# Performance work log

Hardware: AMD Instinct MI355X
Metric: run time of the kernel (lower is better)

The kernel has to match this reference:

```python
import jax, jax.numpy as jnp
import numpy as np

B, N, C, H = 4, 2048, 256, 16
D = C // H  # head dim = 16


def setup_inputs() -> dict:
    key = jax.random.key(0)
    k1, k2, k3 = jax.random.split(key, 3)
    x = jax.random.normal(k1, (B, N, C), dtype=jnp.float32)
    w_qkv = jax.random.normal(k2, (C, 3 * C), dtype=jnp.float32) * (C ** -0.5)
    b_qkv = jnp.zeros((3 * C,), dtype=jnp.float32)
    w_proj = jax.random.normal(k3, (C, C), dtype=jnp.float32) * (C ** -0.5)
    b_proj = jnp.zeros((C,), dtype=jnp.float32)
    return {"x": x, "w_qkv": w_qkv, "b_qkv": b_qkv, "w_proj": w_proj, "b_proj": b_proj}


def reference(x, w_qkv, b_qkv, w_proj, b_proj):
    b, n, c = x.shape
    qkv = x @ w_qkv + b_qkv                       # (B, N, 3C)
    qkv = qkv.reshape(b, n, 3, H, D)
    q = jnp.transpose(qkv[:, :, 0], (0, 2, 1, 3))  # (B, H, N, D)
    k = jnp.transpose(qkv[:, :, 1], (0, 2, 1, 3))
    v = jnp.transpose(qkv[:, :, 2], (0, 2, 1, 3))
    # NOTE: the original module applies NO 1/sqrt(d) scaling.
    attn = jnp.einsum('bhqd,bhkd->bhqk', q, k)     # (B, H, N, N)
    attn = jax.nn.softmax(attn, axis=-1)
    out = jnp.einsum('bhqk,bhkd->bhqd', attn, v)   # (B, H, N, D)
    out = jnp.transpose(out, (0, 2, 1, 3)).reshape(b, n, c)
    return out @ w_proj + b_proj
```

## Files before the change

kernel.cpp:

```cpp
#include <hip/hip_runtime.h>
#include <stdint.h>

typedef __attribute__((ext_vector_type(8))) short short8;
typedef __attribute__((ext_vector_type(4))) short short4v;
typedef __attribute__((ext_vector_type(4))) float float4v;
typedef __attribute__((ext_vector_type(16))) float float16v;
typedef __attribute__((ext_vector_type(4))) uint32_t uint4v;

__device__ __forceinline__ short f2bf(float f) {
    union { float f; uint32_t u; } v; v.f = f;
    uint32_t u = v.u;
    uint32_t r = (u + 0x7fffu + ((u >> 16) & 1u)) >> 16;
    return (short)r;
}

#if __has_builtin(__builtin_amdgcn_cvt_pk_bf16_f32)
typedef __bf16 bf16x2_t __attribute__((ext_vector_type(2)));
__device__ __forceinline__ uint32_t cvt_pk2(float a, float b) {
    union { bf16x2_t v; uint32_t u; } c;
    c.v = __builtin_amdgcn_cvt_pk_bf16_f32(a, b);
    return c.u;
}
#else
__device__ __forceinline__ uint32_t cvt_pk2(float a, float b) {
    union { float f; uint32_t u; } x, y; x.f = a; y.f = b;
    return ((x.u + 0x8000u) >> 16) | ((y.u + 0x8000u) & 0xFFFF0000u);
}
#endif


__global__ __launch_bounds__(256) void cvtW_kernel(const float* __restrict__ wqkv,
                                                   const float* __restrict__ wproj,
                                                   short* __restrict__ outq,
                                                   short* __restrict__ outp) {
    int idx = blockIdx.x * 256 + threadIdx.x;
    if (idx < 196608) {
        int n = idx >> 8, k = idx & 255;
        outq[idx] = f2bf(wqkv[k * 768 + n]);
    } else {
        int i = idx - 196608;
        int n = i >> 8, k = i & 255;
        outp[i] = f2bf(wproj[k * 256 + n]);
    }
}


template<int MODE>
__global__ __launch_bounds__(256) void gemm_kernel(
    const void* __restrict__ Ap, const short* __restrict__ Bt,
    const float* __restrict__ bias,
    short* __restrict__ outQ, short* __restrict__ outK, short* __restrict__ outV,
    float* __restrict__ outP)
{
    const int K = 256;
    int m0 = blockIdx.x * 64;
    int n0 = blockIdx.y * 64;
    int tid = threadIdx.x;
    int wave = tid >> 6, lane = tid & 63, quad = lane >> 4, lc = lane & 15;

    __shared__ __align__(16) short As[64 * 48];
    __shared__ __align__(16) short Bs[64 * 48];

    float4v acc[4];
    #pragma unroll
    for (int t = 0; t < 4; ++t) acc[t] = (float4v){0.f, 0.f, 0.f, 0.f};

    int srow = tid >> 2, sseg = tid & 3;

    for (int c = 0; c < K; c += 32) {
        __syncthreads();
        if (MODE == 0) {
            const float* src = (const float*)Ap + (size_t)(m0 + srow) * K + c + sseg * 8;
            float4 f0 = *(const float4*)src;
            float4 f1 = *(const float4*)(src + 4);
            uint4v u; u.x = cvt_pk2(f0.x, f0.y); u.y = cvt_pk2(f0.z, f0.w);
            u.z = cvt_pk2(f1.x, f1.y); u.w = cvt_pk2(f1.z, f1.w);
            *(uint4v*)(&As[srow * 48 + sseg * 8]) = u;
        } else {
            *(short8*)(&As[srow * 48 + sseg * 8]) =
                *(const short8*)((const short*)Ap + (size_t)(m0 + srow) * K + c + sseg * 8);
        }
        *(short8*)(&Bs[srow * 48 + sseg * 8]) =
            *(const short8*)(Bt + (size_t)(n0 + srow) * K + c + sseg * 8);
        __syncthreads();

        short8 af = *(short8*)(&As[(wave * 16 + lc) * 48 + quad * 8]);
        #pragma unroll
        for (int t = 0; t < 4; ++t) {
            short8 bf = *(short8*)(&Bs[(t * 16 + lc) * 48 + quad * 8]);
            acc[t] = __builtin_amdgcn_mfma_f32_16x16x32_bf16(af, bf, acc[t], 0, 0, 0);
        }
    }

    #pragma unroll
    for (int t = 0; t < 4; ++t) {
        int cg = n0 + t * 16 + lc;
        float bv = bias[cg];
        #pragma unroll
        for (int r = 0; r < 4; ++r) {
            int rg = m0 + wave * 16 + quad * 4 + r;
            float val = acc[t][r] + bv;
            if (MODE == 0) {
                int sq = cg >> 8, rem = cg & 255, h = rem >> 4, d = rem & 15;
                int b = rg >> 11, n = rg & 2047;
                if (sq == 0) val *= 1.4426950408889634f;
                short* dst = (sq == 0) ? outQ : ((sq == 1) ? outK : outV);
                dst[((((size_t)b * 16 + h) * 2048 + n) << 4) + d] = f2bf(val);
            } else {
                outP[(size_t)rg * 256 + cg] = val;
            }
        }
    }
}


__global__ __launch_bounds__(256) void attn_kernel(
    const short* __restrict__ Q, const short* __restrict__ Kp, const short* __restrict__ V,
    short* __restrict__ Out)
{
    const int N = 2048;
    int bh = blockIdx.y;
    int b = bh >> 4, h = bh & 15;
    int tid = threadIdx.x;
    int wave = tid >> 6, lane = tid & 63;
    int m = lane & 31, hi = lane >> 5;
    int qbase = blockIdx.x * 128 + wave * 32;

    const short* Qh = Q + (size_t)bh * N * 16;
    const short* Kh = Kp + (size_t)bh * N * 16;
    const short* Vh = V + (size_t)bh * N * 16;

    __shared__ __align__(16) short Vt[16][264];

    short8 qf = *(const short8*)(Qh + (size_t)(qbase + m) * 16 + hi * 8);

    short8 ones, zeros;
    #pragma unroll
    for (int j = 0; j < 8; ++j) { ones[j] = (short)0x3F80; zeros[j] = 0; }

    float16v Oacc, zf;
    #pragma unroll
    for (int j = 0; j < 16; ++j) { Oacc[j] = 0.f; zf[j] = 0.f; }

    int sd = tid & 15, sa = tid >> 4;
    int kb = ((sa & 1) << 3) | (((sa >> 1) & 1) << 2) | ((sa >> 2) << 4);

    short4v vpack[4];
    #pragma unroll
    for (int cc = 0; cc < 4; ++cc) {
        const short* vp = Vh + (size_t)(cc * 64 + kb) * 16 + sd;
        vpack[cc].x = vp[0]; vpack[cc].y = vp[16];
        vpack[cc].z = vp[32]; vpack[cc].w = vp[48];
    }

    short8 kf1 = *(const short8*)(Kh + (size_t)m * 16 + hi * 8);
    short8 kf2 = *(const short8*)(Kh + (size_t)(32 + m) * 16 + hi * 8);

    for (int sc = 0; sc < N; sc += 256) {
        __syncthreads();
        #pragma unroll
        for (int cc = 0; cc < 4; ++cc)
            *(short4v*)(&Vt[sd][cc * 64 + sa * 4]) = vpack[cc];
        if (sc + 256 < N) {
            #pragma unroll
            for (int cc = 0; cc < 4; ++cc) {
                const short* vp = Vh + (size_t)(sc + 256 + cc * 64 + kb) * 16 + sd;
                vpack[cc].x = vp[0]; vpack[cc].y = vp[16];
                vpack[cc].z = vp[32]; vpack[cc].w = vp[48];
            }
        }
        __syncthreads();

        #pragma unroll
        for (int it = 0; it < 4; ++it) {
            int c = sc + it * 64;
            int cn = (c + 64) & (N - 1);

            float16v S1 = __builtin_amdgcn_mfma_f32_32x32x16_bf16(kf1, qf, zf, 0, 0, 0);
            float16v S2 = __builtin_amdgcn_mfma_f32_32x32x16_bf16(kf2, qf, zf, 0, 0, 0);

            kf1 = *(const short8*)(Kh + (size_t)(cn + m) * 16 + hi * 8);
            kf2 = *(const short8*)(Kh + (size_t)(cn + 32 + m) * 16 + hi * 8);

            union { uint4v u; short8 s; } pA, pB, pC, pD;
            pA.u = (uint4v){
                cvt_pk2(__builtin_amdgcn_exp2f(S1[0]), __builtin_amdgcn_exp2f(S1[1])),
                cvt_pk2(__builtin_amdgcn_exp2f(S1[2]), __builtin_amdgcn_exp2f(S1[3])),
                cvt_pk2(__builtin_amdgcn_exp2f(S1[4]), __builtin_amdgcn_exp2f(S1[5])),
                cvt_pk2(__builtin_amdgcn_exp2f(S1[6]), __builtin_amdgcn_exp2f(S1[7]))};
            pB.u = (uint4v){
                cvt_pk2(__builtin_amdgcn_exp2f(S1[8]),  __builtin_amdgcn_exp2f(S1[9])),
                cvt_pk2(__builtin_amdgcn_exp2f(S1[10]), __builtin_amdgcn_exp2f(S1[11])),
                cvt_pk2(__builtin_amdgcn_exp2f(S1[12]), __builtin_amdgcn_exp2f(S1[13])),
                cvt_pk2(__builtin_amdgcn_exp2f(S1[14]), __builtin_amdgcn_exp2f(S1[15]))};
            pC.u = (uint4v){
                cvt_pk2(__builtin_amdgcn_exp2f(S2[0]), __builtin_amdgcn_exp2f(S2[1])),
                cvt_pk2(__builtin_amdgcn_exp2f(S2[2]), __builtin_amdgcn_exp2f(S2[3])),
                cvt_pk2(__builtin_amdgcn_exp2f(S2[4]), __builtin_amdgcn_exp2f(S2[5])),
                cvt_pk2(__builtin_amdgcn_exp2f(S2[6]), __builtin_amdgcn_exp2f(S2[7]))};
            pD.u = (uint4v){
                cvt_pk2(__builtin_amdgcn_exp2f(S2[8]),  __builtin_amdgcn_exp2f(S2[9])),
                cvt_pk2(__builtin_amdgcn_exp2f(S2[10]), __builtin_amdgcn_exp2f(S2[11])),
                cvt_pk2(__builtin_amdgcn_exp2f(S2[12]), __builtin_amdgcn_exp2f(S2[13])),
                cvt_pk2(__builtin_amdgcn_exp2f(S2[14]), __builtin_amdgcn_exp2f(S2[15]))};

            #pragma unroll
            for (int p = 0; p < 4; ++p) {
                short8 vf;
                if (m < 16)      vf = *(const short8*)(&Vt[m][it * 64 + p * 16 + hi * 8]);
                else if (m == 16) vf = ones;
                else              vf = zeros;
                short8 pf = (p == 0) ? pA.s : (p == 1) ? pB.s : (p == 2) ? pC.s : pD.s;
                Oacc = __builtin_amdgcn_mfma_f32_32x32x16_bf16(vf, pf, Oacc, 0, 0, 0);
            }
        }
    }

    float Lq = __shfl(Oacc[8], m, 64);
    float inv = 1.0f / Lq;
    uint32_t o0 = cvt_pk2(Oacc[0] * inv, Oacc[1] * inv);
    uint32_t o1 = cvt_pk2(Oacc[2] * inv, Oacc[3] * inv);
    uint32_t o2 = cvt_pk2(Oacc[4] * inv, Oacc[5] * inv);
    uint32_t o3 = cvt_pk2(Oacc[6] * inv, Oacc[7] * inv);
    short* row = Out + ((size_t)(b * 2048 + qbase + m)) * 256 + h * 16;
    uint2 w0; w0.x = o0; w0.y = o1;
    uint2 w1; w1.x = o2; w1.y = o3;
    *(uint2*)(row + hi * 4) = w0;
    *(uint2*)(row + 8 + hi * 4) = w1;
}


extern "C" void kernel_launch(void* const* d_in, const int* in_sizes, int n_in,
                              void* d_out, int out_size, void* d_ws, size_t ws_size,
                              hipStream_t stream) {
    const float* x      = (const float*)d_in[0];
    const float* w_qkv  = (const float*)d_in[1];
    const float* b_qkv  = (const float*)d_in[2];
    const float* w_proj = (const float*)d_in[3];
    const float* b_proj = (const float*)d_in[4];
    float* out = (float*)d_out;

    short* wqkvT  = (short*)d_ws;
    short* wprojT = wqkvT + 196608;
    short* Qb     = wprojT + 65536;
    short* Kb     = Qb + 2097152;
    short* Vb     = Kb + 2097152;
    short* Ab     = Vb + 2097152;

    cvtW_kernel<<<1024, 256, 0, stream>>>(w_qkv, w_proj, wqkvT, wprojT);

    gemm_kernel<0><<<dim3(128, 12), 256, 0, stream>>>(x, wqkvT, b_qkv, Qb, Kb, Vb, nullptr);

    attn_kernel<<<dim3(16, 64), 256, 0, stream>>>(Qb, Kb, Vb, Ab);

    gemm_kernel<1><<<dim3(128, 4), 256, 0, stream>>>(Ab, wprojT, b_proj,
                                                     nullptr, nullptr, nullptr, out);
}
```

Baseline: 132.9 us.

## Split attention key range across two wave groups and reduce partial outputs in LDS

The attention block grows to 512 threads, with two groups of four waves each processing half of the key sequence for the same 128 queries. The partial outputs and row sums are combined through shared memory before normalisation. The ones/zeros rows of the V tile are now stored in LDS instead of being chosen per lane, which removes branching in the inner loop. This doubles the waves per block to hide latency, at the cost of an extra reduction, more LDS, and two more barriers.

```diff
diff --git a/kernel.cpp b/kernel.cpp
--- a/kernel.cpp
+++ b/kernel.cpp
@@ -114,57 +114,64 @@
 }
 
 
-__global__ __launch_bounds__(256) void attn_kernel(
+__global__ __launch_bounds__(512, 8) void attn_kernel(
     const short* __restrict__ Q, const short* __restrict__ Kp, const short* __restrict__ V,
     short* __restrict__ Out)
 {
-    const int N = 2048;
+    const int NH = 1024;
     int bh = blockIdx.y;
     int b = bh >> 4, h = bh & 15;
     int tid = threadIdx.x;
     int wave = tid >> 6, lane = tid & 63;
     int m = lane & 31, hi = lane >> 5;
-    int qbase = blockIdx.x * 128 + wave * 32;
-
-    const short* Qh = Q + (size_t)bh * N * 16;
-    const short* Kh = Kp + (size_t)bh * N * 16;
-    const short* Vh = V + (size_t)bh * N * 16;
-
-    __shared__ __align__(16) short Vt[16][264];
+    int grp = wave >> 2;
+    int koff = grp << 10;
+    int qbase = blockIdx.x * 128 + (wave & 3) * 32;
+
+    const short* Qh = Q + (size_t)bh * 2048 * 16;
+    const short* Kh = Kp + (size_t)bh * 2048 * 16;
+    const short* Vh = V + (size_t)bh * 2048 * 16;
+
+    __shared__ __align__(16) short Vt[2][32][264];
+
+    for (int idx = tid; idx < 2 * 16 * 264; idx += 512) {
+        int buf = idx / (16 * 264);
+        int rem = idx - buf * (16 * 264);
+        int row = 16 + rem / 264;
+        int col = rem - (row - 16) * 264;
+        Vt[buf][row][col] = (row == 16) ? (short)0x3F80 : (short)0;
+    }
 
     short8 qf = *(const short8*)(Qh + (size_t)(qbase + m) * 16 + hi * 8);
 
-    short8 ones, zeros;
-    #pragma unroll
-    for (int j = 0; j < 8; ++j) { ones[j] = (short)0x3F80; zeros[j] = 0; }
-
     float16v Oacc, zf;
     #pragma unroll
     for (int j = 0; j < 16; ++j) { Oacc[j] = 0.f; zf[j] = 0.f; }
 
-    int sd = tid & 15, sa = tid >> 4;
+    int t8 = tid & 255;
+    int sd = t8 & 15, sa = t8 >> 4;
     int kb = ((sa & 1) << 3) | (((sa >> 1) & 1) << 2) | ((sa >> 2) << 4);
 
     short4v vpack[4];
     #pragma unroll
     for (int cc = 0; cc < 4; ++cc) {
-        const short* vp = Vh + (size_t)(cc * 64 + kb) * 16 + sd;
+        const short* vp = Vh + (size_t)(koff + cc * 64 + kb) * 16 + sd;
         vpack[cc].x = vp[0]; vpack[cc].y = vp[16];
         vpack[cc].z = vp[32]; vpack[cc].w = vp[48];
     }
 
-    short8 kf1 = *(const short8*)(Kh + (size_t)m * 16 + hi * 8);
-    short8 kf2 = *(const short8*)(Kh + (size_t)(32 + m) * 16 + hi * 8);
-
-    for (int sc = 0; sc < N; sc += 256) {
+    short8 kf1 = *(const short8*)(Kh + (size_t)(koff + m) * 16 + hi * 8);
+    short8 kf2 = *(const short8*)(Kh + (size_t)(koff + 32 + m) * 16 + hi * 8);
+
+    for (int sc = 0; sc < NH; sc += 256) {
         __syncthreads();
         #pragma unroll
         for (int cc = 0; cc < 4; ++cc)
-            *(short4v*)(&Vt[sd][cc * 64 + sa * 4]) = vpack[cc];
-        if (sc + 256 < N) {
+            *(short4v*)(&Vt[grp][sd][cc * 64 + sa * 4]) = vpack[cc];
+        if (sc + 256 < NH) {
             #pragma unroll
             for (int cc = 0; cc < 4; ++cc) {
-                const short* vp = Vh + (size_t)(sc + 256 + cc * 64 + kb) * 16 + sd;
+                const short* vp = Vh + (size_t)(koff + sc + 256 + cc * 64 + kb) * 16 + sd;
                 vpack[cc].x = vp[0]; vpack[cc].y = vp[16];
                 vpack[cc].z = vp[32]; vpack[cc].w = vp[48];
             }
@@ -174,13 +181,13 @@
         #pragma unroll
         for (int it = 0; it < 4; ++it) {
             int c = sc + it * 64;
-            int cn = (c + 64) & (N - 1);
+            int cn = (c + 64) & (NH - 1);
 
             float16v S1 = __builtin_amdgcn_mfma_f32_32x32x16_bf16(kf1, qf, zf, 0, 0, 0);
             float16v S2 = __builtin_amdgcn_mfma_f32_32x32x16_bf16(kf2, qf, zf, 0, 0, 0);
 
-            kf1 = *(const short8*)(Kh + (size_t)(cn + m) * 16 + hi * 8);
-            kf2 = *(const short8*)(Kh + (size_t)(cn + 32 + m) * 16 + hi * 8);
+            kf1 = *(const short8*)(Kh + (size_t)(koff + cn + m) * 16 + hi * 8);
+            kf2 = *(const short8*)(Kh + (size_t)(koff + cn + 32 + m) * 16 + hi * 8);
 
             union { uint4v u; short8 s; } pA, pB, pC, pD;
             pA.u = (uint4v){
@@ -206,27 +213,43 @@
 
             #pragma unroll
             for (int p = 0; p < 4; ++p) {
-                short8 vf;
-                if (m < 16)      vf = *(const short8*)(&Vt[m][it * 64 + p * 16 + hi * 8]);
-                else if (m == 16) vf = ones;
-                else              vf = zeros;
+                short8 vf = *(short8*)(&Vt[grp][m][it * 64 + p * 16 + hi * 8]);
                 short8 pf = (p == 0) ? pA.s : (p == 1) ? pB.s : (p == 2) ? pC.s : pD.s;
                 Oacc = __builtin_amdgcn_mfma_f32_32x32x16_bf16(vf, pf, Oacc, 0, 0, 0);
             }
         }
     }
 
-    float Lq = __shfl(Oacc[8], m, 64);
-    float inv = 1.0f / Lq;
-    uint32_t o0 = cvt_pk2(Oacc[0] * inv, Oacc[1] * inv);
-    uint32_t o1 = cvt_pk2(Oacc[2] * inv, Oacc[3] * inv);
-    uint32_t o2 = cvt_pk2(Oacc[4] * inv, Oacc[5] * inv);
-    uint32_t o3 = cvt_pk2(Oacc[6] * inv, Oacc[7] * inv);
-    short* row = Out + ((size_t)(b * 2048 + qbase + m)) * 256 + h * 16;
-    uint2 w0; w0.x = o0; w0.y = o1;
-    uint2 w1; w1.x = o2; w1.y = o3;
-    *(uint2*)(row + hi * 4) = w0;
-    *(uint2*)(row + 8 + hi * 4) = w1;
+    __syncthreads();
+    float* cb = (float*)&Vt[0][0][0];
+    if (wave >= 4) {
+        int base = ((wave - 4) * 64 + lane) * 12;
+        *(float4v*)(cb + base)     = (float4v){Oacc[0], Oacc[1], Oacc[2], Oacc[3]};
+        *(float4v*)(cb + base + 4) = (float4v){Oacc[4], Oacc[5], Oacc[6], Oacc[7]};
+        cb[base + 8] = Oacc[8];
+    }
+    __syncthreads();
+    if (wave < 4) {
+        int base = (wave * 64 + lane) * 12;
+        float4v p0 = *(float4v*)(cb + base);
+        float4v p1 = *(float4v*)(cb + base + 4);
+        float Lp = cb[base + 8];
+        Oacc[0] += p0[0]; Oacc[1] += p0[1]; Oacc[2] += p0[2]; Oacc[3] += p0[3];
+        Oacc[4] += p1[0]; Oacc[5] += p1[1]; Oacc[6] += p1[2]; Oacc[7] += p1[3];
+        Oacc[8] += Lp;
+
+        float Lq = __shfl(Oacc[8], m, 64);
+        float inv = 1.0f / Lq;
+        uint32_t o0 = cvt_pk2(Oacc[0] * inv, Oacc[1] * inv);
+        uint32_t o1 = cvt_pk2(Oacc[2] * inv, Oacc[3] * inv);
+        uint32_t o2 = cvt_pk2(Oacc[4] * inv, Oacc[5] * inv);
+        uint32_t o3 = cvt_pk2(Oacc[6] * inv, Oacc[7] * inv);
+        short* row = Out + ((size_t)(b * 2048 + qbase + m)) * 256 + h * 16;
+        uint2 w0; w0.x = o0; w0.y = o1;
+        uint2 w1; w1.x = o2; w1.y = o3;
+        *(uint2*)(row + hi * 4) = w0;
+        *(uint2*)(row + 8 + hi * 4) = w1;
+    }
 }
 
 
@@ -251,7 +274,7 @@
 
     gemm_kernel<0><<<dim3(128, 12), 256, 0, stream>>>(x, wqkvT, b_qkv, Qb, Kb, Vb, nullptr);
 
-    attn_kernel<<<dim3(16, 64), 256, 0, stream>>>(Qb, Kb, Vb, Ab);
+    attn_kernel<<<dim3(16, 64), 512, 0, stream>>>(Qb, Kb, Vb, Ab);
 
     gemm_kernel<1><<<dim3(128, 4), 256, 0, stream>>>(Ab, wprojT, b_proj,
                                                      nullptr, nullptr, nullptr, out);
```

New measurement: 176.3 us. 32.7% more time.

## Split attention over the key dimension and add a combine kernel

Applied to the files above, without the earlier changes.

The attention kernel now splits the 2048 keys into two halves across blockIdx.z, which doubles the block count to 2048. Each split writes unnormalized fp32 partial outputs and row sums to workspace. A new combine kernel adds the two halves, normalizes, and writes the bf16 attention output. The ones/zeros rows for the row-sum trick now come from shared memory instead of per-lane branches. In exchange it adds an extra launch and roughly 18 MB of fp32 partial traffic. Summing without a running max is safe because the original code also has no max subtraction.

```diff
diff --git a/kernel.cpp b/kernel.cpp
--- a/kernel.cpp
+++ b/kernel.cpp
@@ -116,27 +116,29 @@
 
 __global__ __launch_bounds__(256) void attn_kernel(
     const short* __restrict__ Q, const short* __restrict__ Kp, const short* __restrict__ V,
-    short* __restrict__ Out)
+    float* __restrict__ Pout, float* __restrict__ Lout)
 {
-    const int N = 2048;
+    const int NH = 1024;
     int bh = blockIdx.y;
-    int b = bh >> 4, h = bh & 15;
+    int split = blockIdx.z;
     int tid = threadIdx.x;
     int wave = tid >> 6, lane = tid & 63;
     int m = lane & 31, hi = lane >> 5;
     int qbase = blockIdx.x * 128 + wave * 32;
 
-    const short* Qh = Q + (size_t)bh * N * 16;
-    const short* Kh = Kp + (size_t)bh * N * 16;
-    const short* Vh = V + (size_t)bh * N * 16;
-
-    __shared__ __align__(16) short Vt[16][264];
+    const short* Qh = Q + (size_t)bh * 2048 * 16;
+    const short* Kh = Kp + ((size_t)bh * 2048 + (split << 10)) * 16;
+    const short* Vh = V + ((size_t)bh * 2048 + (split << 10)) * 16;
+
+    __shared__ __align__(16) short Vt[32][264];
+
+    for (int idx = tid; idx < 16 * 264; idx += 256) {
+        int row = 16 + idx / 264;
+        int col = idx - (row - 16) * 264;
+        Vt[row][col] = (row == 16) ? (short)0x3F80 : (short)0;
+    }
 
     short8 qf = *(const short8*)(Qh + (size_t)(qbase + m) * 16 + hi * 8);
-
-    short8 ones, zeros;
-    #pragma unroll
-    for (int j = 0; j < 8; ++j) { ones[j] = (short)0x3F80; zeros[j] = 0; }
 
     float16v Oacc, zf;
     #pragma unroll
@@ -156,12 +158,12 @@
     short8 kf1 = *(const short8*)(Kh + (size_t)m * 16 + hi * 8);
     short8 kf2 = *(const short8*)(Kh + (size_t)(32 + m) * 16 + hi * 8);
 
-    for (int sc = 0; sc < N; sc += 256) {
+    for (int sc = 0; sc < NH; sc += 256) {
         __syncthreads();
         #pragma unroll
         for (int cc = 0; cc < 4; ++cc)
             *(short4v*)(&Vt[sd][cc * 64 + sa * 4]) = vpack[cc];
-        if (sc + 256 < N) {
+        if (sc + 256 < NH) {
             #pragma unroll
             for (int cc = 0; cc < 4; ++cc) {
                 const short* vp = Vh + (size_t)(sc + 256 + cc * 64 + kb) * 16 + sd;
@@ -174,7 +176,7 @@
         #pragma unroll
         for (int it = 0; it < 4; ++it) {
             int c = sc + it * 64;
-            int cn = (c + 64) & (N - 1);
+            int cn = (c + 64) & (NH - 1);
 
             float16v S1 = __builtin_amdgcn_mfma_f32_32x32x16_bf16(kf1, qf, zf, 0, 0, 0);
             float16v S2 = __builtin_amdgcn_mfma_f32_32x32x16_bf16(kf2, qf, zf, 0, 0, 0);
@@ -206,27 +208,52 @@
 
             #pragma unroll
             for (int p = 0; p < 4; ++p) {
-                short8 vf;
-                if (m < 16)      vf = *(const short8*)(&Vt[m][it * 64 + p * 16 + hi * 8]);
-                else if (m == 16) vf = ones;
-                else              vf = zeros;
+                short8 vf = *(short8*)(&Vt[m][it * 64 + p * 16 + hi * 8]);
                 short8 pf = (p == 0) ? pA.s : (p == 1) ? pB.s : (p == 2) ? pC.s : pD.s;
                 Oacc = __builtin_amdgcn_mfma_f32_32x32x16_bf16(vf, pf, Oacc, 0, 0, 0);
             }
         }
     }
 
-    float Lq = __shfl(Oacc[8], m, 64);
-    float inv = 1.0f / Lq;
-    uint32_t o0 = cvt_pk2(Oacc[0] * inv, Oacc[1] * inv);
-    uint32_t o1 = cvt_pk2(Oacc[2] * inv, Oacc[3] * inv);
-    uint32_t o2 = cvt_pk2(Oacc[4] * inv, Oacc[5] * inv);
-    uint32_t o3 = cvt_pk2(Oacc[6] * inv, Oacc[7] * inv);
-    short* row = Out + ((size_t)(b * 2048 + qbase + m)) * 256 + h * 16;
-    uint2 w0; w0.x = o0; w0.y = o1;
-    uint2 w1; w1.x = o2; w1.y = o3;
-    *(uint2*)(row + hi * 4) = w0;
-    *(uint2*)(row + 8 + hi * 4) = w1;
+    size_t qi = (size_t)bh * 2048 + qbase + m;
+    float* pb = Pout + ((size_t)split * 131072 + qi) * 16;
+    *(float4v*)(pb + hi * 4)     = (float4v){Oacc[0], Oacc[1], Oacc[2], Oacc[3]};
+    *(float4v*)(pb + 8 + hi * 4) = (float4v){Oacc[4], Oacc[5], Oacc[6], Oacc[7]};
+    if (hi == 0) Lout[(size_t)split * 131072 + qi] = Oacc[8];
+}
+
+
+__global__ __launch_bounds__(256) void combine_kernel(const float* __restrict__ P,
+                                                      const float* __restrict__ Lb,
+                                                      short* __restrict__ Ab) {
+    int idx = blockIdx.x * 256 + threadIdx.x;
+    int h = idx & 15;
+    int bn = idx >> 4;
+    int b = bn >> 11;
+    size_t qi = ((size_t)(b * 16 + h)) * 2048 + (bn & 2047);
+    const float* p0 = P + qi * 16;
+    const float* p1 = P + (qi + 131072) * 16;
+    float inv = 1.0f / (Lb[qi] + Lb[qi + 131072]);
+    float4v a0 = *(const float4v*)(p0);
+    float4v a1 = *(const float4v*)(p0 + 4);
+    float4v a2 = *(const float4v*)(p0 + 8);
+    float4v a3 = *(const float4v*)(p0 + 12);
+    float4v c0 = *(const float4v*)(p1);
+    float4v c1 = *(const float4v*)(p1 + 4);
+    float4v c2 = *(const float4v*)(p1 + 8);
+    float4v c3 = *(const float4v*)(p1 + 12);
+    uint4v o0, o1;
+    o0.x = cvt_pk2((a0[0] + c0[0]) * inv, (a0[1] + c0[1]) * inv);
+    o0.y = cvt_pk2((a0[2] + c0[2]) * inv, (a0[3] + c0[3]) * inv);
+    o0.z = cvt_pk2((a1[0] + c1[0]) * inv, (a1[1] + c1[1]) * inv);
+    o0.w = cvt_pk2((a1[2] + c1[2]) * inv, (a1[3] + c1[3]) * inv);
+    o1.x = cvt_pk2((a2[0] + c2[0]) * inv, (a2[1] + c2[1]) * inv);
+    o1.y = cvt_pk2((a2[2] + c2[2]) * inv, (a2[3] + c2[3]) * inv);
+    o1.z = cvt_pk2((a3[0] + c3[0]) * inv, (a3[1] + c3[1]) * inv);
+    o1.w = cvt_pk2((a3[2] + c3[2]) * inv, (a3[3] + c3[3]) * inv);
+    short* row = Ab + (size_t)bn * 256 + h * 16;
+    *(uint4v*)(row)     = o0;
+    *(uint4v*)(row + 8) = o1;
 }
 
 
@@ -246,12 +273,16 @@
     short* Kb     = Qb + 2097152;
     short* Vb     = Kb + 2097152;
     short* Ab     = Vb + 2097152;
+    float* Pp     = (float*)(Ab + 2097152);
+    float* Lp     = Pp + 4194304;
 
     cvtW_kernel<<<1024, 256, 0, stream>>>(w_qkv, w_proj, wqkvT, wprojT);
 
     gemm_kernel<0><<<dim3(128, 12), 256, 0, stream>>>(x, wqkvT, b_qkv, Qb, Kb, Vb, nullptr);
 
-    attn_kernel<<<dim3(16, 64), 256, 0, stream>>>(Qb, Kb, Vb, Ab);
+    attn_kernel<<<dim3(16, 64, 2), 256, 0, stream>>>(Qb, Kb, Vb, Pp, Lp);
+
+    combine_kernel<<<512, 256, 0, stream>>>(Pp, Lp, Ab);
 
     gemm_kernel<1><<<dim3(128, 4), 256, 0, stream>>>(Ab, wprojT, b_proj,
                                                      nullptr, nullptr, nullptr, out);
```

New measurement: 143.2 us. +7.7%, slower.

## Rewrite projection GEMMs with larger swizzled tiles and async LDS loads

Applied to the files above, without the earlier changes.

Both projection GEMMs are replaced by a kernel with 128-wide N tiles (TM 128 or 64 on M), K steps of 64, XOR-swizzled shared memory, and global_load_lds direct-to-LDS loads. This raises data reuse per block and cuts the number of barrier rounds. Because x must now arrive as bf16, its conversion moves into the weight-conversion kernel, which adds an extra pass over x in global memory. The attention kernel also puts the ones/zeros rows for V in LDS, so the per-lane branch in the PV MFMA loop goes away, at the cost of more shared memory.

```diff
diff --git a/kernel.cpp b/kernel.cpp
--- a/kernel.cpp
+++ b/kernel.cpp
@@ -28,86 +28,125 @@
 }
 #endif
 
+__device__ __forceinline__ void async_ld16(short* lds, const short* g) {
+    __builtin_amdgcn_global_load_lds(
+        (const __attribute__((address_space(1))) void*)g,
+        (__attribute__((address_space(3))) void*)lds, 16, 0, 0);
+}
+
 
 __global__ __launch_bounds__(256) void cvtW_kernel(const float* __restrict__ wqkv,
                                                    const float* __restrict__ wproj,
+                                                   const float* __restrict__ x,
                                                    short* __restrict__ outq,
-                                                   short* __restrict__ outp) {
-    int idx = blockIdx.x * 256 + threadIdx.x;
-    if (idx < 196608) {
-        int n = idx >> 8, k = idx & 255;
-        outq[idx] = f2bf(wqkv[k * 768 + n]);
+                                                   short* __restrict__ outp,
+                                                   short* __restrict__ xb) {
+    int gid = blockIdx.x * 256 + threadIdx.x;
+    if (gid < 262144) {
+        const float* src = x + (size_t)gid * 8;
+        float4 f0 = *(const float4*)src;
+        float4 f1 = *(const float4*)(src + 4);
+        uint4v u; u.x = cvt_pk2(f0.x, f0.y); u.y = cvt_pk2(f0.z, f0.w);
+        u.z = cvt_pk2(f1.x, f1.y); u.w = cvt_pk2(f1.z, f1.w);
+        *(uint4v*)(xb + (size_t)gid * 8) = u;
     } else {
-        int i = idx - 196608;
-        int n = i >> 8, k = i & 255;
-        outp[i] = f2bf(wproj[k * 256 + n]);
-    }
-}
-
-
-template<int MODE>
-__global__ __launch_bounds__(256) void gemm_kernel(
-    const void* __restrict__ Ap, const short* __restrict__ Bt,
+        int idx = gid - 262144;
+        if (idx < 196608) {
+            int n = idx >> 8, k = idx & 255;
+            outq[idx] = f2bf(wqkv[k * 768 + n]);
+        } else {
+            int i = idx - 196608;
+            int n = i >> 8, k = i & 255;
+            outp[i] = f2bf(wproj[k * 256 + n]);
+        }
+    }
+}
+
+
+template<int TM, int MODE>
+__global__ __launch_bounds__(256) void gemm2_kernel(
+    const short* __restrict__ A, const short* __restrict__ Bt,
     const float* __restrict__ bias,
     short* __restrict__ outQ, short* __restrict__ outK, short* __restrict__ outV,
     float* __restrict__ outP)
 {
     const int K = 256;
-    int m0 = blockIdx.x * 64;
-    int n0 = blockIdx.y * 64;
+    const int MI = TM / 32;
     int tid = threadIdx.x;
-    int wave = tid >> 6, lane = tid & 63, quad = lane >> 4, lc = lane & 15;
-
-    __shared__ __align__(16) short As[64 * 48];
-    __shared__ __align__(16) short Bs[64 * 48];
-
-    float4v acc[4];
-    #pragma unroll
-    for (int t = 0; t < 4; ++t) acc[t] = (float4v){0.f, 0.f, 0.f, 0.f};
-
-    int srow = tid >> 2, sseg = tid & 3;
-
-    for (int c = 0; c < K; c += 32) {
-        __syncthreads();
-        if (MODE == 0) {
-            const float* src = (const float*)Ap + (size_t)(m0 + srow) * K + c + sseg * 8;
-            float4 f0 = *(const float4*)src;
-            float4 f1 = *(const float4*)(src + 4);
-            uint4v u; u.x = cvt_pk2(f0.x, f0.y); u.y = cvt_pk2(f0.z, f0.w);
-            u.z = cvt_pk2(f1.x, f1.y); u.w = cvt_pk2(f1.z, f1.w);
-            *(uint4v*)(&As[srow * 48 + sseg * 8]) = u;
-        } else {
-            *(short8*)(&As[srow * 48 + sseg * 8]) =
-                *(const short8*)((const short*)Ap + (size_t)(m0 + srow) * K + c + sseg * 8);
-        }
-        *(short8*)(&Bs[srow * 48 + sseg * 8]) =
-            *(const short8*)(Bt + (size_t)(n0 + srow) * K + c + sseg * 8);
-        __syncthreads();
-
-        short8 af = *(short8*)(&As[(wave * 16 + lc) * 48 + quad * 8]);
-        #pragma unroll
-        for (int t = 0; t < 4; ++t) {
-            short8 bf = *(short8*)(&Bs[(t * 16 + lc) * 48 + quad * 8]);
-            acc[t] = __builtin_amdgcn_mfma_f32_16x16x32_bf16(af, bf, acc[t], 0, 0, 0);
-        }
-    }
-
-    #pragma unroll
-    for (int t = 0; t < 4; ++t) {
-        int cg = n0 + t * 16 + lc;
-        float bv = bias[cg];
-        #pragma unroll
-        for (int r = 0; r < 4; ++r) {
-            int rg = m0 + wave * 16 + quad * 4 + r;
-            float val = acc[t][r] + bv;
-            if (MODE == 0) {
-                int sq = cg >> 8, rem = cg & 255, h = rem >> 4, d = rem & 15;
-                int b = rg >> 11, n = rg & 2047;
-                if (sq == 0) val *= 1.4426950408889634f;
-                short* dst = (sq == 0) ? outQ : ((sq == 1) ? outK : outV);
-                dst[((((size_t)b * 16 + h) * 2048 + n) << 4) + d] = f2bf(val);
-            } else {
-                outP[(size_t)rg * 256 + cg] = val;
+    int w = tid >> 6, lane = tid & 63;
+    int wr = w >> 1, wc = w & 1;
+    int quad = lane >> 4, lc = lane & 15;
+    int m0 = blockIdx.x * TM, n0 = blockIdx.y * 128;
+
+    __shared__ __align__(16) short As[TM * 64];
+    __shared__ __align__(16) short Bs[128 * 64];
+
+    float4v acc[MI][4];
+    #pragma unroll
+    for (int i = 0; i < MI; ++i)
+        #pragma unroll
+        for (int j = 0; j < 4; ++j) acc[i][j] = (float4v){0.f, 0.f, 0.f, 0.f};
+
+    int l8 = lane >> 3, l7 = lane & 7;
+    int scol = ((l7 ^ l8) * 8);
+
+    for (int kt = 0; kt < 4; ++kt) {
+        int c = kt * 64;
+        __syncthreads();
+        #pragma unroll
+        for (int i = 0; i < TM / 32; ++i) {
+            int row = i * 32 + w * 8 + l8;
+            async_ld16(&As[row * 64 + l7 * 8],
+                       A + (size_t)(m0 + row) * K + c + scol);
+        }
+        #pragma unroll
+        for (int i = 0; i < 4; ++i) {
+            int row = i * 32 + w * 8 + l8;
+            async_ld16(&Bs[row * 64 + l7 * 8],
+                       Bt + (size_t)(n0 + row) * K + c + scol);
+        }
+        __syncthreads();
+
+        #pragma unroll
+        for (int ks = 0; ks < 2; ++ks) {
+            short8 af[MI], bf[4];
+            #pragma unroll
+            for (int i = 0; i < MI; ++i) {
+                int r = wr * (TM / 2) + i * 16 + lc;
+                af[i] = *(short8*)(&As[r * 64 + (((ks * 4 + quad) ^ (r & 7)) * 8)]);
+            }
+            #pragma unroll
+            for (int j = 0; j < 4; ++j) {
+                int r = wc * 64 + j * 16 + lc;
+                bf[j] = *(short8*)(&Bs[r * 64 + (((ks * 4 + quad) ^ (r & 7)) * 8)]);
+            }
+            #pragma unroll
+            for (int i = 0; i < MI; ++i)
+                #pragma unroll
+                for (int j = 0; j < 4; ++j)
+                    acc[i][j] = __builtin_amdgcn_mfma_f32_16x16x32_bf16(af[i], bf[j], acc[i][j], 0, 0, 0);
+        }
+    }
+
+    #pragma unroll
+    for (int i = 0; i < MI; ++i) {
+        #pragma unroll
+        for (int j = 0; j < 4; ++j) {
+            int cg = n0 + wc * 64 + j * 16 + lc;
+            float bv = bias[cg];
+            #pragma unroll
+            for (int r = 0; r < 4; ++r) {
+                int rg = m0 + wr * (TM / 2) + i * 16 + quad * 4 + r;
+                float val = acc[i][j][r] + bv;
+                if (MODE == 0) {
+                    int sq = cg >> 8, rem = cg & 255, h = rem >> 4, d = rem & 15;
+                    int b = rg >> 11, n = rg & 2047;
+                    if (sq == 0) val *= 1.4426950408889634f;
+                    short* dst = (sq == 0) ? outQ : ((sq == 1) ? outK : outV);
+                    dst[((((size_t)b * 16 + h) * 2048 + n) << 4) + d] = f2bf(val);
+                } else {
+                    outP[(size_t)rg * 256 + cg] = val;
+                }
             }
         }
     }
@@ -130,13 +169,15 @@
     const short* Kh = Kp + (size_t)bh * N * 16;
     const short* Vh = V + (size_t)bh * N * 16;
 
-    __shared__ __align__(16) short Vt[16][264];
+    __shared__ __align__(16) short Vt[32][264];
+
+    for (int idx = tid; idx < 16 * 264; idx += 256) {
+        int row = 16 + idx / 264;
+        int col = idx - (row - 16) * 264;
+        Vt[row][col] = (row == 16) ? (short)0x3F80 : (short)0;
+    }
 
     short8 qf = *(const short8*)(Qh + (size_t)(qbase + m) * 16 + hi * 8);
-
-    short8 ones, zeros;
-    #pragma unroll
-    for (int j = 0; j < 8; ++j) { ones[j] = (short)0x3F80; zeros[j] = 0; }
 
     float16v Oacc, zf;
     #pragma unroll
@@ -206,10 +247,7 @@
 
             #pragma unroll
             for (int p = 0; p < 4; ++p) {
-                short8 vf;
-                if (m < 16)      vf = *(const short8*)(&Vt[m][it * 64 + p * 16 + hi * 8]);
-                else if (m == 16) vf = ones;
-                else              vf = zeros;
+                short8 vf = *(short8*)(&Vt[m][it * 64 + p * 16 + hi * 8]);
                 short8 pf = (p == 0) ? pA.s : (p == 1) ? pB.s : (p == 2) ? pC.s : pD.s;
                 Oacc = __builtin_amdgcn_mfma_f32_32x32x16_bf16(vf, pf, Oacc, 0, 0, 0);
             }
@@ -242,17 +280,19 @@
 
     short* wqkvT  = (short*)d_ws;
     short* wprojT = wqkvT + 196608;
-    short* Qb     = wprojT + 65536;
+    short* xb     = wprojT + 65536;
+    short* Qb     = xb + 2097152;
     short* Kb     = Qb + 2097152;
     short* Vb     = Kb + 2097152;
     short* Ab     = Vb + 2097152;
 
-    cvtW_kernel<<<1024, 256, 0, stream>>>(w_qkv, w_proj, wqkvT, wprojT);
-
-    gemm_kernel<0><<<dim3(128, 12), 256, 0, stream>>>(x, wqkvT, b_qkv, Qb, Kb, Vb, nullptr);
+    cvtW_kernel<<<2048, 256, 0, stream>>>(w_qkv, w_proj, x, wqkvT, wprojT, xb);
+
+    gemm2_kernel<128, 0><<<dim3(64, 6), 256, 0, stream>>>(xb, wqkvT, b_qkv,
+                                                          Qb, Kb, Vb, nullptr);
 
     attn_kernel<<<dim3(16, 64), 256, 0, stream>>>(Qb, Kb, Vb, Ab);
 
-    gemm_kernel<1><<<dim3(128, 4), 256, 0, stream>>>(Ab, wprojT, b_proj,
-                                                     nullptr, nullptr, nullptr, out);
-}
+    gemm2_kernel<64, 1><<<dim3(128, 2), 256, 0, stream>>>(Ab, wprojT, b_proj,
+                                                          nullptr, nullptr, nullptr, out);
+}
```

Measured after the change: 136.2 us. 1.02x slower.
